# Optimization experiments

Measured on AMD Instinct MI355X. Metric: run time of the kernel, lower is better.

Reference implementation:

```python
import jax, jax.numpy as jnp
import numpy as np

B, C, H, W = 256, 1024, 7, 7
D_HID, N_CLS = 768, 5

def setup_inputs() -> dict:
    key = jax.random.key(0)
    k1, k2, k3, k4, k5 = jax.random.split(key, 5)
    flat = C * H * W  # 50176
    return {
        "features": jax.random.normal(k1, (B, C, H, W), dtype=jnp.float32),
        "W1": jax.random.normal(k2, (D_HID, flat), dtype=jnp.float32) * 0.02,
        "b1": jax.random.normal(k3, (D_HID,), dtype=jnp.float32) * 0.02,
        "W2": jax.random.normal(k4, (N_CLS, D_HID), dtype=jnp.float32) * 0.02,
        "b2": jax.random.normal(k5, (N_CLS,), dtype=jnp.float32) * 0.02,
    }

def reference(features, W1, b1, W2, b2):
    # PCAM: per-(batch, channel) global max over spatial dims, broadcast-multiplied
    # back onto the feature map. Replaces the torch Python double loop with one
    # fused reduce-max + elementwise multiply.
    ch_max = jnp.max(features, axis=(2, 3), keepdims=True)  # [B, C, 1, 1]
    pcams = features * ch_max                               # [B, C, H, W]
    flat = pcams.reshape(pcams.shape[0], -1)                # [B, C*H*W]
    h = jax.nn.relu(flat @ W1.T + b1)                       # [B, 768]
    logits = h @ W2.T + b2                                  # [B, num_classes]
    return (logits, features)
```

## Files before the change

### kernel.cpp

```cpp
#include <hip/hip_runtime.h>
#include <hip/hip_bf16.h>

#define B_SZ   256
#define C_SZ   1024
#define HW     49
#define KDIM   50176
#define DHID   768
#define NCLS   5

typedef __bf16 bf16x8 __attribute__((ext_vector_type(8)));
typedef float  f32x4  __attribute__((ext_vector_type(4)));

#define GLOAD_LDS16(gsrc, ldst) \
  __builtin_amdgcn_global_load_lds((__attribute__((address_space(1))) void*)(gsrc), \
                                   (__attribute__((address_space(3))) void*)(ldst), 16, 0, 0)

__global__ __launch_bounds__(256) void pcam_kernel(const float* __restrict__ feat,
                                                   float* __restrict__ feat_out,
                                                   __bf16* __restrict__ pcam) {
  __shared__ float sv[1568];
  __shared__ float smax[32];
  const int tid = threadIdx.x;
  const size_t base = (size_t)blockIdx.x * 1568;

  const float4* src4 = (const float4*)(feat + base);
  float4* dst4 = (float4*)(feat_out + base);
  #pragma unroll
  for (int i = 0; i < 2; ++i) {
    int idx = tid + i * 256;
    if (idx < 392) {
      float4 v = src4[idx];
      dst4[idx] = v;
      ((float4*)sv)[idx] = v;
    }
  }
  __syncthreads();

  {
    const int r = tid >> 3, p = tid & 7;
    float mx = -INFINITY;
    for (int i = p; i < HW; i += 8) mx = fmaxf(mx, sv[r * HW + i]);
    #pragma unroll
    for (int off = 1; off < 8; off <<= 1) mx = fmaxf(mx, __shfl_xor(mx, off));
    if (p == 0) smax[r] = mx;
  }
  __syncthreads();

  for (int i = tid; i < 1568; i += 256) {
    int r = (i * 1338) >> 16;
    float v = sv[i] * smax[r];
    pcam[base + i] = (__bf16)v;
  }
}

#define BM 128
#define BN 128
#define BK 32
#define NBUF 3
#define MT 2
#define NT 6
#define KSPLIT 42
#define KSTEPS 1568

__global__ __launch_bounds__(512, 4) void gemm1_kernel(const __bf16* __restrict__ pcam,
                                                       const float* __restrict__ W1,
                                                       float* __restrict__ h_part) {
  __shared__ __bf16 Asm[NBUF][BM * BK];
  __shared__ float  Bsm[NBUF][BN * BK];

  const int tid  = threadIdx.x;
  const int lane = tid & 63;
  const int w    = tid >> 6;
  const int wm   = w >> 2;
  const int wn   = w & 3;
  const int bx   = blockIdx.x;
  const int m0   = (bx & 1) * BM;
  const int n0   = (bx >> 1) * BN;
  const int ks   = blockIdx.y;
  const int s0   = (ks * KSTEPS) / KSPLIT;
  const int s1   = ((ks + 1) * KSTEPS) / KSPLIT;

  const int m_d = w * 16 + (lane >> 2);
  const int ua  = (lane & 3) ^ (m_d & 3);
  const __bf16* asrc = pcam + (size_t)(m0 + m_d) * KDIM + ua * 8;

  const int r1  = w * 8 + (lane >> 3);
  const int ub  = (lane & 7) ^ (r1 & 7);
  const float* bsrc1 = W1 + (size_t)(n0 + r1) * KDIM + ub * 4;
  const float* bsrc2 = W1 + (size_t)(n0 + 64 + r1) * KDIM + ub * 4;

  char* aw = (char*)&Asm[0][0] + w * 1024;
  char* bw = (char*)&Bsm[0][0] + w * 1024;

  f32x4 acc[4][2];
  #pragma unroll
  for (int i = 0; i < 4; ++i)
    #pragma unroll
    for (int j = 0; j < 2; ++j) acc[i][j] = f32x4{0.f, 0.f, 0.f, 0.f};

#define ISSUE(bi, s) do { \
    const size_t ko_ = (size_t)(s) * BK; \
    GLOAD_LDS16(asrc + ko_,  aw + (size_t)(bi) * (BM * BK * 2)); \
    GLOAD_LDS16(bsrc1 + ko_, bw + (size_t)(bi) * (BN * BK * 4)); \
    GLOAD_LDS16(bsrc2 + ko_, bw + (size_t)(bi) * (BN * BK * 4) + 8192); \
  } while (0)

#define COMPUTE(bi) do { \
    const int j_  = lane >> 4; \
    const int c_  = lane & 15; \
    bf16x8 af[4]; \
    _Pragma("unroll") \
    for (int i = 0; i < 4; ++i) { \
      const int m = wm * 64 + i * 16 + c_; \
      af[i] = *(const bf16x8*)((const char*)Asm[bi] + m * 64 + ((j_ ^ (m & 3)) << 4)); \
    } \
    bf16x8 bfr[2]; \
    _Pragma("unroll") \
    for (int jf = 0; jf < 2; ++jf) { \
      const int n = wn * 32 + jf * 16 + c_; \
      const f32x4 b0 = *(const f32x4*)((const char*)Bsm[bi] + n * 128 + (((2 * j_)     ^ (n & 7)) << 4)); \
      const f32x4 b1 = *(const f32x4*)((const char*)Bsm[bi] + n * 128 + (((2 * j_ + 1) ^ (n & 7)) << 4)); \
      bfr[jf][0] = (__bf16)b0[0]; bfr[jf][1] = (__bf16)b0[1]; \
      bfr[jf][2] = (__bf16)b0[2]; bfr[jf][3] = (__bf16)b0[3]; \
      bfr[jf][4] = (__bf16)b1[0]; bfr[jf][5] = (__bf16)b1[1]; \
      bfr[jf][6] = (__bf16)b1[2]; bfr[jf][7] = (__bf16)b1[3]; \
    } \
    _Pragma("unroll") \
    for (int i = 0; i < 4; ++i) \
      _Pragma("unroll") \
      for (int jf = 0; jf < 2; ++jf) \
        acc[i][jf] = __builtin_amdgcn_mfma_f32_16x16x32_bf16(af[i], bfr[jf], acc[i][jf], 0, 0, 0); \
  } while (0)

  int b0i = 0, b1i = 1, b2i = 2;
  ISSUE(0, s0);
  if (s0 + 1 < s1) ISSUE(1, s0 + 1);

  for (int s = s0; s < s1; ++s) {
    if (s + 2 < s1) {
      ISSUE(b2i, s + 2);
      asm volatile("s_waitcnt vmcnt(6)" ::: "memory");
    } else if (s + 1 < s1) {
      asm volatile("s_waitcnt vmcnt(3)" ::: "memory");
    } else {
      asm volatile("s_waitcnt vmcnt(0)" ::: "memory");
    }
    __builtin_amdgcn_s_barrier();
    COMPUTE(b0i);
    asm volatile("s_waitcnt lgkmcnt(0)" ::: "memory");
    __builtin_amdgcn_s_barrier();
    const int t = b0i; b0i = b1i; b1i = b2i; b2i = t;
  }

  float* out = h_part + (size_t)ks * DHID * B_SZ;
  #pragma unroll
  for (int i = 0; i < 4; ++i) {
    const int mb = m0 + wm * 64 + i * 16 + (lane >> 4) * 4;
    #pragma unroll
    for (int j = 0; j < 2; ++j) {
      const int n = n0 + wn * 32 + j * 16 + (lane & 15);
      *(f32x4*)(out + (size_t)n * B_SZ + mb) = acc[i][j];
    }
  }
#undef ISSUE
#undef COMPUTE
}

__global__ __launch_bounds__(256) void reduce_kernel(const float* __restrict__ h_part,
                                                     const float* __restrict__ b1,
                                                     float* __restrict__ h) {
  const int n = blockIdx.x;
  const int m = threadIdx.x;
  float s = 0.f;
  #pragma unroll 6
  for (int ks = 0; ks < KSPLIT; ++ks)
    s += h_part[((size_t)ks * DHID + n) * B_SZ + m];
  float v = s + b1[n];
  h[(size_t)m * DHID + n] = v > 0.f ? v : 0.f;
}

__global__ __launch_bounds__(64) void head_kernel(const float* __restrict__ h,
                                                  const float* __restrict__ W2,
                                                  const float* __restrict__ b2,
                                                  float* __restrict__ logits) {
  const int m = blockIdx.x;
  const int lane = threadIdx.x;
  float hv[12];
  #pragma unroll
  for (int j = 0; j < 12; ++j) hv[j] = h[(size_t)m * DHID + j * 64 + lane];
  #pragma unroll
  for (int c = 0; c < NCLS; ++c) {
    float s = 0.f;
    #pragma unroll
    for (int j = 0; j < 12; ++j) s += hv[j] * W2[c * DHID + j * 64 + lane];
    #pragma unroll
    for (int off = 32; off > 0; off >>= 1) s += __shfl_xor(s, off);
    if (lane == 0) logits[m * NCLS + c] = s + b2[c];
  }
}

extern "C" void kernel_launch(void* const* d_in, const int* in_sizes, int n_in,
                              void* d_out, int out_size, void* d_ws, size_t ws_size,
                              hipStream_t stream) {
  const float* feat = (const float*)d_in[0];
  const float* W1   = (const float*)d_in[1];
  const float* b1   = (const float*)d_in[2];
  const float* W2   = (const float*)d_in[3];
  const float* b2   = (const float*)d_in[4];

  float* logits   = (float*)d_out;
  float* feat_out = (float*)d_out + (size_t)B_SZ * NCLS;

  char* ws = (char*)d_ws;
  __bf16* pcam   = (__bf16*)ws;
  float*  h_part = (float*)(ws + (size_t)B_SZ * KDIM * 2);
  float*  h      = (float*)(ws + (size_t)B_SZ * KDIM * 2
                               + (size_t)KSPLIT * DHID * B_SZ * 4);

  pcam_kernel<<<(B_SZ * C_SZ) / 32, 256, 0, stream>>>(feat, feat_out, pcam);
  gemm1_kernel<<<dim3(MT * NT, KSPLIT), 512, 0, stream>>>(pcam, W1, h_part);
  reduce_kernel<<<DHID, 256, 0, stream>>>(h_part, b1, h);
  head_kernel<<<B_SZ, 64, 0, stream>>>(h, W2, b2, logits);
}
```

Measured before the change: 110.4 us.

## Retile GEMM1 to full-batch 256x64x64 tiles and halve split-K

The GEMM1 tile changes from 128x128x32 to 256x64x64, so each block covers the whole batch. W1, the dominant fp32 stream, is then read exactly once instead of twice across M tiles. Split-K drops from 42 to 21, which halves the partial-sum traffic and the work in the reduce kernel. The grid shrinks to 252 blocks at occupancy 2, with more LDS per stage and reworked swizzled load offsets. This risks fewer waves in flight and less latency hiding.

```diff
diff --git a/kernel.cpp b/kernel.cpp
--- a/kernel.cpp
+++ b/kernel.cpp
@@ -53,16 +53,17 @@
   }
 }
 
-#define BM 128
-#define BN 128
-#define BK 32
+#define BM 256
+#define BN 64
+#define BK 64
 #define NBUF 3
-#define MT 2
-#define NT 6
-#define KSPLIT 42
-#define KSTEPS 1568
-
-__global__ __launch_bounds__(512, 4) void gemm1_kernel(const __bf16* __restrict__ pcam,
+#define NT 12
+#define KSPLIT 21
+#define KSTEPS 784
+#define ASZ (BM * BK * 2)
+#define BSZ (BN * BK * 4)
+
+__global__ __launch_bounds__(512, 2) void gemm1_kernel(const __bf16* __restrict__ pcam,
                                                        const float* __restrict__ W1,
                                                        float* __restrict__ h_part) {
   __shared__ __bf16 Asm[NBUF][BM * BK];
@@ -73,63 +74,66 @@
   const int w    = tid >> 6;
   const int wm   = w >> 2;
   const int wn   = w & 3;
-  const int bx   = blockIdx.x;
-  const int m0   = (bx & 1) * BM;
-  const int n0   = (bx >> 1) * BN;
+  const int n0   = blockIdx.x * BN;
   const int ks   = blockIdx.y;
   const int s0   = (ks * KSTEPS) / KSPLIT;
   const int s1   = ((ks + 1) * KSTEPS) / KSPLIT;
 
-  const int m_d = w * 16 + (lane >> 2);
-  const int ua  = (lane & 3) ^ (m_d & 3);
-  const __bf16* asrc = pcam + (size_t)(m0 + m_d) * KDIM + ua * 8;
-
-  const int r1  = w * 8 + (lane >> 3);
-  const int ub  = (lane & 7) ^ (r1 & 7);
-  const float* bsrc1 = W1 + (size_t)(n0 + r1) * KDIM + ub * 4;
-  const float* bsrc2 = W1 + (size_t)(n0 + 64 + r1) * KDIM + ub * 4;
-
-  char* aw = (char*)&Asm[0][0] + w * 1024;
-  char* bw = (char*)&Bsm[0][0] + w * 1024;
-
-  f32x4 acc[4][2];
-  #pragma unroll
-  for (int i = 0; i < 4; ++i)
-    #pragma unroll
-    for (int j = 0; j < 2; ++j) acc[i][j] = f32x4{0.f, 0.f, 0.f, 0.f};
+  unsigned a_off0, a_off1, a_off2, a_off3;
+  {
+    unsigned ug, m;
+    ug = (w * 4 + 0) * 64 + lane; m = ug >> 3; a_off0 = m * (unsigned)KDIM + (((ug & 7) ^ (m & 7)) * 8u);
+    ug = (w * 4 + 1) * 64 + lane; m = ug >> 3; a_off1 = m * (unsigned)KDIM + (((ug & 7) ^ (m & 7)) * 8u);
+    ug = (w * 4 + 2) * 64 + lane; m = ug >> 3; a_off2 = m * (unsigned)KDIM + (((ug & 7) ^ (m & 7)) * 8u);
+    ug = (w * 4 + 3) * 64 + lane; m = ug >> 3; a_off3 = m * (unsigned)KDIM + (((ug & 7) ^ (m & 7)) * 8u);
+  }
+  unsigned b_off0, b_off1;
+  {
+    unsigned ug, r, up;
+    ug = (w * 2 + 0) * 64 + lane; r = ug >> 4; up = ug & 15;
+    b_off0 = (unsigned)(n0 + r) * (unsigned)KDIM + (((up >> 1) ^ (r & 7)) * 8u) + ((up & 1) * 4u);
+    ug = (w * 2 + 1) * 64 + lane; r = ug >> 4; up = ug & 15;
+    b_off1 = (unsigned)(n0 + r) * (unsigned)KDIM + (((up >> 1) ^ (r & 7)) * 8u) + ((up & 1) * 4u);
+  }
+
+  f32x4 acc[8];
+  #pragma unroll
+  for (int i = 0; i < 8; ++i) acc[i] = f32x4{0.f, 0.f, 0.f, 0.f};
 
 #define ISSUE(bi, s) do { \
-    const size_t ko_ = (size_t)(s) * BK; \
-    GLOAD_LDS16(asrc + ko_,  aw + (size_t)(bi) * (BM * BK * 2)); \
-    GLOAD_LDS16(bsrc1 + ko_, bw + (size_t)(bi) * (BN * BK * 4)); \
-    GLOAD_LDS16(bsrc2 + ko_, bw + (size_t)(bi) * (BN * BK * 4) + 8192); \
+    const unsigned ka = (unsigned)(s) * BK; \
+    GLOAD_LDS16(pcam + a_off0 + ka, (char*)Asm + (size_t)(bi) * ASZ + (w * 4 + 0) * 1024); \
+    GLOAD_LDS16(pcam + a_off1 + ka, (char*)Asm + (size_t)(bi) * ASZ + (w * 4 + 1) * 1024); \
+    GLOAD_LDS16(pcam + a_off2 + ka, (char*)Asm + (size_t)(bi) * ASZ + (w * 4 + 2) * 1024); \
+    GLOAD_LDS16(pcam + a_off3 + ka, (char*)Asm + (size_t)(bi) * ASZ + (w * 4 + 3) * 1024); \
+    GLOAD_LDS16(W1 + b_off0 + ka,   (char*)Bsm + (size_t)(bi) * BSZ + (w * 2 + 0) * 1024); \
+    GLOAD_LDS16(W1 + b_off1 + ka,   (char*)Bsm + (size_t)(bi) * BSZ + (w * 2 + 1) * 1024); \
   } while (0)
 
 #define COMPUTE(bi) do { \
-    const int j_  = lane >> 4; \
-    const int c_  = lane & 15; \
-    bf16x8 af[4]; \
+    const int j_ = lane >> 4; \
+    const int c_ = lane & 15; \
     _Pragma("unroll") \
-    for (int i = 0; i < 4; ++i) { \
-      const int m = wm * 64 + i * 16 + c_; \
-      af[i] = *(const bf16x8*)((const char*)Asm[bi] + m * 64 + ((j_ ^ (m & 3)) << 4)); \
+    for (int ksub = 0; ksub < 2; ++ksub) { \
+      bf16x8 af[8]; \
+      _Pragma("unroll") \
+      for (int i = 0; i < 8; ++i) { \
+        const int m = wm * 128 + i * 16 + c_; \
+        const int u = ksub * 4 + j_; \
+        af[i] = *(const bf16x8*)((const char*)Asm + (size_t)(bi) * ASZ + m * 128 + ((u ^ (m & 7)) << 4)); \
+      } \
+      const int r  = wn * 16 + c_; \
+      const int g  = ksub * 4 + j_; \
+      const int gp = g ^ (r & 7); \
+      const f32x4 v0 = *(const f32x4*)((const char*)Bsm + (size_t)(bi) * BSZ + r * 256 + gp * 32); \
+      const f32x4 v1 = *(const f32x4*)((const char*)Bsm + (size_t)(bi) * BSZ + r * 256 + gp * 32 + 16); \
+      bf16x8 bf; \
+      bf[0] = (__bf16)v0[0]; bf[1] = (__bf16)v0[1]; bf[2] = (__bf16)v0[2]; bf[3] = (__bf16)v0[3]; \
+      bf[4] = (__bf16)v1[0]; bf[5] = (__bf16)v1[1]; bf[6] = (__bf16)v1[2]; bf[7] = (__bf16)v1[3]; \
+      _Pragma("unroll") \
+      for (int i = 0; i < 8; ++i) \
+        acc[i] = __builtin_amdgcn_mfma_f32_16x16x32_bf16(af[i], bf, acc[i], 0, 0, 0); \
     } \
-    bf16x8 bfr[2]; \
-    _Pragma("unroll") \
-    for (int jf = 0; jf < 2; ++jf) { \
-      const int n = wn * 32 + jf * 16 + c_; \
-      const f32x4 b0 = *(const f32x4*)((const char*)Bsm[bi] + n * 128 + (((2 * j_)     ^ (n & 7)) << 4)); \
-      const f32x4 b1 = *(const f32x4*)((const char*)Bsm[bi] + n * 128 + (((2 * j_ + 1) ^ (n & 7)) << 4)); \
-      bfr[jf][0] = (__bf16)b0[0]; bfr[jf][1] = (__bf16)b0[1]; \
-      bfr[jf][2] = (__bf16)b0[2]; bfr[jf][3] = (__bf16)b0[3]; \
-      bfr[jf][4] = (__bf16)b1[0]; bfr[jf][5] = (__bf16)b1[1]; \
-      bfr[jf][6] = (__bf16)b1[2]; bfr[jf][7] = (__bf16)b1[3]; \
-    } \
-    _Pragma("unroll") \
-    for (int i = 0; i < 4; ++i) \
-      _Pragma("unroll") \
-      for (int jf = 0; jf < 2; ++jf) \
-        acc[i][jf] = __builtin_amdgcn_mfma_f32_16x16x32_bf16(af[i], bfr[jf], acc[i][jf], 0, 0, 0); \
   } while (0)
 
   int b0i = 0, b1i = 1, b2i = 2;
@@ -139,9 +143,9 @@
   for (int s = s0; s < s1; ++s) {
     if (s + 2 < s1) {
       ISSUE(b2i, s + 2);
+      asm volatile("s_waitcnt vmcnt(12)" ::: "memory");
+    } else if (s + 1 < s1) {
       asm volatile("s_waitcnt vmcnt(6)" ::: "memory");
-    } else if (s + 1 < s1) {
-      asm volatile("s_waitcnt vmcnt(3)" ::: "memory");
     } else {
       asm volatile("s_waitcnt vmcnt(0)" ::: "memory");
     }
@@ -154,13 +158,10 @@
 
   float* out = h_part + (size_t)ks * DHID * B_SZ;
   #pragma unroll
-  for (int i = 0; i < 4; ++i) {
-    const int mb = m0 + wm * 64 + i * 16 + (lane >> 4) * 4;
-    #pragma unroll
-    for (int j = 0; j < 2; ++j) {
-      const int n = n0 + wn * 32 + j * 16 + (lane & 15);
-      *(f32x4*)(out + (size_t)n * B_SZ + mb) = acc[i][j];
-    }
+  for (int i = 0; i < 8; ++i) {
+    const int mb = wm * 128 + i * 16 + (lane >> 4) * 4;
+    const int n  = n0 + wn * 16 + (lane & 15);
+    *(f32x4*)(out + (size_t)n * B_SZ + mb) = acc[i];
   }
 #undef ISSUE
 #undef COMPUTE
@@ -172,7 +173,7 @@
   const int n = blockIdx.x;
   const int m = threadIdx.x;
   float s = 0.f;
-  #pragma unroll 6
+  #pragma unroll
   for (int ks = 0; ks < KSPLIT; ++ks)
     s += h_part[((size_t)ks * DHID + n) * B_SZ + m];
   float v = s + b1[n];
@@ -218,7 +219,7 @@
                                + (size_t)KSPLIT * DHID * B_SZ * 4);
 
   pcam_kernel<<<(B_SZ * C_SZ) / 32, 256, 0, stream>>>(feat, feat_out, pcam);
-  gemm1_kernel<<<dim3(MT * NT, KSPLIT), 512, 0, stream>>>(pcam, W1, h_part);
+  gemm1_kernel<<<dim3(NT, KSPLIT), 512, 0, stream>>>(pcam, W1, h_part);
   reduce_kernel<<<DHID, 256, 0, stream>>>(h_part, b1, h);
   head_kernel<<<B_SZ, 64, 0, stream>>>(h, W2, b2, logits);
 }
```

New measurement: 106.8 us. 3.2% less time.
